# Kernel tuning notes

Hardware: AMD Instinct MI355X
Metric: run time of the kernel (lower is better)

Reference implementation:

```python
import jax, jax.numpy as jnp
import numpy as np

N_NODES = 100000
N_EDGES = 1600000
N_GRAPHS = 256
HIDDEN = 256
ADD_FEATURES = 7
BN_EPS = 1e-5


def setup_inputs() -> dict:
    key = jax.random.key(0)
    ks = jax.random.split(key, 12)
    x = jax.random.normal(ks[0], (N_NODES, 1), dtype=jnp.float32)
    edge_index = jax.random.randint(ks[1], (2, N_EDGES), 0, N_NODES, dtype=jnp.int32)
    batch = jnp.sort(jax.random.randint(ks[2], (N_NODES,), 0, N_GRAPHS, dtype=jnp.int32))
    y_feat = jax.random.normal(ks[3], (N_GRAPHS, ADD_FEATURES), dtype=jnp.float32)
    # learned parameters
    W_conv = jax.random.normal(ks[4], (1, HIDDEN), dtype=jnp.float32) * 0.5
    b_conv = jnp.zeros((HIDDEN,), dtype=jnp.float32)
    gamma = jnp.ones((HIDDEN,), dtype=jnp.float32)
    beta = jnp.zeros((HIDDEN,), dtype=jnp.float32)
    W1 = jax.random.normal(ks[5], (HIDDEN + ADD_FEATURES, 128), dtype=jnp.float32) * (1.0 / np.sqrt(HIDDEN + ADD_FEATURES))
    b1 = jnp.zeros((128,), dtype=jnp.float32)
    W2 = jax.random.normal(ks[6], (128, 2), dtype=jnp.float32) * (1.0 / np.sqrt(128))
    b2 = jnp.zeros((2,), dtype=jnp.float32)
    return {"x": x, "edge_index": edge_index, "batch": batch, "y_feat": y_feat,
            "W_conv": W_conv, "b_conv": b_conv, "gamma": gamma, "beta": beta,
            "W1": W1, "b1": b1, "W2": W2, "b2": b2}


def _gcn_conv(x, W, b, edge_index, n_nodes):
    # PyG GCNConv: add self-loops, symmetric normalization D^-1/2 (A+I) D^-1/2 (x W) + b
    loop = jnp.arange(n_nodes, dtype=edge_index.dtype)
    src = jnp.concatenate([edge_index[0], loop])
    dst = jnp.concatenate([edge_index[1], loop])
    deg = jax.ops.segment_sum(jnp.ones_like(dst, dtype=x.dtype), dst, num_segments=n_nodes)
    dinv = jnp.where(deg > 0, jax.lax.rsqrt(jnp.maximum(deg, 1e-12)), 0.0)
    norm = dinv[src] * dinv[dst]                      # [E+N]
    xw = x @ W                                        # [N, H]
    msg = xw[src] * norm[:, None]                     # gather [E+N, H]
    return jax.ops.segment_sum(msg, dst, num_segments=n_nodes) + b


def reference(x, edge_index, batch, y_feat, W_conv, b_conv, gamma, beta, W1, b1, W2, b2):
    n_nodes = x.shape[0]
    h = _gcn_conv(x, W_conv, b_conv, edge_index, n_nodes)      # [N, 256]
    h = jax.nn.gelu(h, approximate=False)
    # BatchNorm over nodes (training-mode batch stats, biased variance, eps=1e-5)
    mean = jnp.mean(h, axis=0)
    var = jnp.mean(jnp.square(h - mean), axis=0)
    h = (h - mean) * jax.lax.rsqrt(var + BN_EPS) * gamma + beta
    # global mean pool by graph id
    sums = jax.ops.segment_sum(h, batch, num_segments=N_GRAPHS)           # [G, 256]
    counts = jax.ops.segment_sum(jnp.ones((n_nodes,), h.dtype), batch, num_segments=N_GRAPHS)
    pooled = sums / jnp.maximum(counts, 1.0)[:, None]
    g = jnp.concatenate([pooled, y_feat], axis=1)               # [G, 263]
    g = jax.nn.gelu(g @ W1 + b1, approximate=False)             # [G, 128]
    out = jax.nn.sigmoid(g @ W2 + b2)                           # [G, 2]
    return out
```

## Files before the change

### kernel.cpp

```cpp
#include <hip/hip_runtime.h>
#include <hip/hip_bf16.h>

#define HID 256
#define ADDF 7
#define MLP1 128
#define BN_EPS 1e-5f
#define NREP 8

#define NB 512
#define BW 196
#define BCAP 4096
#define PC 2048
#define NW 4

__device__ __forceinline__ float gelu_fast(float z) {
    float z2 = z * z;
    float y2 = z * fmaf(0.07135481627f, z2, 1.59576912161f);
    float u  = __expf(fminf(y2, 80.0f));
    return z * u * __builtin_amdgcn_rcpf(u + 1.0f);
}

__global__ __launch_bounds__(256) void k_hist(
        const int* __restrict__ dst, int* __restrict__ hist,
        float* __restrict__ zbase, int zcount, int E, int nchunk, int cpx) {
    __shared__ int h[NW][NB];
    const int t = threadIdx.x;
    const int bid = blockIdx.x;

    int gt = bid * 256 + t;
    if (gt < zcount) zbase[gt] = 0.0f;

    const int m = (bid & 7) * cpx + (bid >> 3);
    for (int k = t; k < NW * NB; k += 256) (&h[0][0])[k] = 0;
    __syncthreads();

    if (m < nchunk) {
        const int s0 = m * PC;
        const int e0 = min(s0 + PC, E);
        const int w = t >> 6;
        const bool al = ((((uintptr_t)(dst + s0)) & 15) == 0);
        const int n4 = al ? ((e0 - s0) >> 2) : 0;
        const int4* dst4 = (const int4*)(dst + s0);
        for (int q = t; q < n4; q += 256) {
            int4 d = dst4[q];
            atomicAdd(&h[w][d.x / BW], 1);
            atomicAdd(&h[w][d.y / BW], 1);
            atomicAdd(&h[w][d.z / BW], 1);
            atomicAdd(&h[w][d.w / BW], 1);
        }
        for (int i = s0 + (n4 << 2) + t; i < e0; i += 256)
            atomicAdd(&h[w][dst[i] / BW], 1);
        __syncthreads();
        for (int b = t; b < NB; b += 256)
            hist[(size_t)m * NB + b] = h[0][b] + h[1][b] + h[2][b] + h[3][b];
    }
}

__global__ __launch_bounds__(64) void k_scan(
        int* __restrict__ hist, int* __restrict__ binCur,
        const int* __restrict__ batch, int* __restrict__ cnt,
        int nchunk, int N, int G) {
    const int bin = blockIdx.x;
    const int lane = threadIdx.x;
    __shared__ int bounds[2];

    if (bin < G && lane < 2) {
        int target = bin + lane;
        int lo = 0, hi = N;
        while (lo < hi) { int mid = (lo + hi) >> 1; if (batch[mid] < target) lo = mid + 1; else hi = mid; }
        bounds[lane] = lo;
    }

    const int per = (nchunk + 63) / 64;
    const int m0 = lane * per;
    const int m1 = min(m0 + per, nchunk);
    int sum = 0;
    for (int m = m0; m < m1; ++m) sum += hist[(size_t)m * NB + bin];

    int incl = sum;
    #pragma unroll
    for (int d = 1; d < 64; d <<= 1) {
        int o = __shfl_up(incl, d);
        if (lane >= d) incl += o;
    }
    const int total = __shfl(incl, 63);
    int run = bin * BCAP + (incl - sum);
    for (int m = m0; m < m1; ++m) {
        int c = hist[(size_t)m * NB + bin];
        hist[(size_t)m * NB + bin] = run;
        run += c;
    }
    if (lane == 63) binCur[bin] = bin * BCAP + total;

    __syncthreads();
    if (bin < G && lane == 0) cnt[bin] = bounds[1] - bounds[0];
}

__global__ __launch_bounds__(256) void k_store(
        const int* __restrict__ src, const int* __restrict__ dst,
        const int* __restrict__ hist, int* __restrict__ recs,
        int E, int nchunk, int cpx) {
    __shared__ int cur[NB];
    const int t = threadIdx.x;
    const int m = ((int)blockIdx.x & 7) * cpx + ((int)blockIdx.x >> 3);
    if (m >= nchunk) return;

    for (int b = t; b < NB; b += 256) cur[b] = hist[(size_t)m * NB + b];
    __syncthreads();

    const int s0 = m * PC;
    const int e0 = min(s0 + PC, E);
    const bool al = (((((uintptr_t)(dst + s0)) | ((uintptr_t)(src + s0))) & 15) == 0);
    const int n4 = al ? ((e0 - s0) >> 2) : 0;
    const int4* dst4 = (const int4*)(dst + s0);
    const int4* src4 = (const int4*)(src + s0);
    for (int q = t; q < n4; q += 256) {
        int4 d = dst4[q];
        int4 s = src4[q];
        int bin, pos;
        bin = d.x / BW; pos = atomicAdd(&cur[bin], 1); recs[pos] = ((d.x - bin * BW) << 17) | s.x;
        bin = d.y / BW; pos = atomicAdd(&cur[bin], 1); recs[pos] = ((d.y - bin * BW) << 17) | s.y;
        bin = d.z / BW; pos = atomicAdd(&cur[bin], 1); recs[pos] = ((d.z - bin * BW) << 17) | s.z;
        bin = d.w / BW; pos = atomicAdd(&cur[bin], 1); recs[pos] = ((d.w - bin * BW) << 17) | s.w;
    }
    for (int i = s0 + (n4 << 2) + t; i < e0; i += 256) {
        int d = dst[i];
        int bin = d / BW;
        int pos = atomicAdd(&cur[bin], 1);
        recs[pos] = ((d - bin * BW) << 17) | src[i];
    }
}

__global__ __launch_bounds__(512) void k_degv(
        const int* __restrict__ recs, const int* __restrict__ binCur,
        const float* __restrict__ x, float* __restrict__ dinv, float* __restrict__ v, int N) {
    __shared__ int degL[BW];
    const int b = blockIdx.x;
    const int t = threadIdx.x;
    if (t < BW) degL[t] = 0;
    __syncthreads();

    const int start = b * BCAP;
    const int end   = binCur[b];
    const int n4 = (end - start) >> 2;
    const int4* r4 = (const int4*)(recs + start);
    for (int q = t; q < n4; q += 512) {
        int4 r = r4[q];
        atomicAdd(&degL[r.x >> 17], 1);
        atomicAdd(&degL[r.y >> 17], 1);
        atomicAdd(&degL[r.z >> 17], 1);
        atomicAdd(&degL[r.w >> 17], 1);
    }
    for (int i = start + (n4 << 2) + t; i < end; i += 512)
        atomicAdd(&degL[recs[i] >> 17], 1);
    __syncthreads();

    int node = b * BW + t;
    if (t < BW && node < N) {
        float di = rsqrtf((float)degL[t] + 1.0f);
        dinv[node] = di;
        v[node]    = di * x[node];
    }
}

__global__ __launch_bounds__(512) void k_agg_gelu(
        const int* __restrict__ recs, const int* __restrict__ binCur,
        const float* __restrict__ v, const float* __restrict__ dinv,
        const int* __restrict__ batch,
        const float* __restrict__ Wc, const float* __restrict__ bc,
        float* __restrict__ Sgj, float* __restrict__ Trep, float* __restrict__ T2rep, int N) {
    __shared__ float aggL[BW];
    __shared__ float sh_s[BW];
    __shared__ int   sh_b[BW];
    const int b = blockIdx.x;
    const int t = threadIdx.x;
    if (t < BW) aggL[t] = 0.0f;
    __syncthreads();

    const int start = b * BCAP;
    const int end   = binCur[b];
    const int n4 = (end - start) >> 2;
    const int4* r4 = (const int4*)(recs + start);
    for (int q = t; q < n4; q += 512) {
        int4 r = r4[q];
        atomicAdd(&aggL[r.x >> 17], v[r.x & 0x1FFFF]);
        atomicAdd(&aggL[r.y >> 17], v[r.y & 0x1FFFF]);
        atomicAdd(&aggL[r.z >> 17], v[r.z & 0x1FFFF]);
        atomicAdd(&aggL[r.w >> 17], v[r.w & 0x1FFFF]);
    }
    for (int i = start + (n4 << 2) + t; i < end; i += 512) {
        int rec = recs[i];
        atomicAdd(&aggL[rec >> 17], v[rec & 0x1FFFF]);
    }
    __syncthreads();

    const int node0 = b * BW;
    const int count = min(BW, N - node0);
    if (count <= 0) return;

    if (t < count) {
        int node = node0 + t;
        sh_s[t] = dinv[node] * (aggL[t] + v[node]);
        sh_b[t] = batch[node];
    }
    __syncthreads();

    const int f = t & 255;
    const int nbeg = (t < 256) ? 0 : 98;
    const int nend = (t < 256) ? min(98, count) : count;
    if (nbeg < nend) {
        const float wa = Wc[f];
        const float wb = bc[f];
        float tsum = 0.f, t2sum = 0.f, gsum = 0.f;
        int gid = sh_b[nbeg];
        int n = nbeg;
        for (; n + 2 <= nend; n += 2) {
            float h0 = gelu_fast(fmaf(sh_s[n],     wa, wb));
            float h1 = gelu_fast(fmaf(sh_s[n + 1], wa, wb));
            int b0 = sh_b[n], b1v = sh_b[n + 1];
            tsum += h0 + h1; t2sum += fmaf(h0, h0, h1 * h1);
            if (b0 != gid)  { atomicAdd(&Sgj[gid * HID + f], gsum); gsum = 0.f; gid = b0; }
            gsum += h0;
            if (b1v != gid) { atomicAdd(&Sgj[gid * HID + f], gsum); gsum = 0.f; gid = b1v; }
            gsum += h1;
        }
        if (n < nend) {
            float h0 = gelu_fast(fmaf(sh_s[n], wa, wb));
            tsum += h0; t2sum += h0 * h0;
            int b0 = sh_b[n];
            if (b0 != gid) { atomicAdd(&Sgj[gid * HID + f], gsum); gsum = 0.f; gid = b0; }
            gsum += h0;
        }
        atomicAdd(&Sgj[gid * HID + f], gsum);
        const int r = b & (NREP - 1);
        atomicAdd(&Trep [r * HID + f], tsum);
        atomicAdd(&T2rep[r * HID + f], t2sum);
    }
}

__global__ __launch_bounds__(HID) void k_pool_mlp(
        const float* __restrict__ Sgj, const float* __restrict__ Trep, const float* __restrict__ T2rep,
        const int* __restrict__ cnt, const float* __restrict__ gamma, const float* __restrict__ beta,
        const float* __restrict__ yfeat,
        const float* __restrict__ W1, const float* __restrict__ b1,
        const float* __restrict__ W2, const float* __restrict__ b2,
        float* __restrict__ out, int N) {
    __shared__ float gv[HID + ADDF];
    __shared__ float hid[MLP1];
    const int g = blockIdx.x;
    const int t = threadIdx.x;

    float Ts = 0.f, T2s = 0.f;
    #pragma unroll
    for (int r = 0; r < NREP; ++r) { Ts += Trep[r * HID + t]; T2s += T2rep[r * HID + t]; }
    float invN = 1.0f / (float)N;
    float mean = Ts * invN;
    float var  = fmaf(-mean, mean, T2s * invN);
    float rinv = rsqrtf(var + BN_EPS);
    float c = (float)max(cnt[g], 1);
    gv[t] = (Sgj[g * HID + t] / c - mean) * rinv * gamma[t] + beta[t];
    if (t < ADDF) gv[HID + t] = yfeat[g * ADDF + t];
    __syncthreads();

    if (t < MLP1) {
        float acc = b1[t];
        #pragma unroll 8
        for (int k = 0; k < HID + ADDF; ++k)
            acc = fmaf(gv[k], W1[k * MLP1 + t], acc);
        hid[t] = gelu_fast(acc);
    }
    __syncthreads();

    if (t < 2) {
        float o = b2[t];
        for (int k = 0; k < MLP1; ++k)
            o = fmaf(hid[k], W2[k * 2 + t], o);
        out[g * 2 + t] = 1.0f / (1.0f + expf(-o));
    }
}

__global__ void k_init_fb(float* zp, int nz, const int* __restrict__ batch,
                          int* __restrict__ cnt, int N, int G) {
    const int nzBlocks = (nz + 255) / 256;
    if ((int)blockIdx.x < nzBlocks) {
        int i = blockIdx.x * 256 + threadIdx.x;
        if (i < nz) zp[i] = 0.0f;
    } else {
        const int t = threadIdx.x;
        if (t < G) {
            int lo = 0, hi = N;
            while (lo < hi) { int mid = (lo + hi) >> 1; if (batch[mid] < t) lo = mid + 1; else hi = mid; }
            int start = lo;
            lo = 0; hi = N;
            while (lo < hi) { int mid = (lo + hi) >> 1; if (batch[mid] < t + 1) lo = mid + 1; else hi = mid; }
            cnt[t] = lo - start;
        }
    }
}
__global__ void k_zero(float* p, int n) {
    for (int i = blockIdx.x * blockDim.x + threadIdx.x; i < n; i += gridDim.x * blockDim.x)
        p[i] = 0.0f;
}
__global__ void k_deg_fb(const int* __restrict__ dst, float* __restrict__ deg, int E) {
    int i = blockIdx.x * blockDim.x + threadIdx.x;
    if (i < E) atomicAdd(&deg[dst[i]], 1.0f);
}
__global__ void k_dinv_fb(float* __restrict__ deg, const float* __restrict__ x,
                          float* __restrict__ v, int N) {
    int i = blockIdx.x * blockDim.x + threadIdx.x;
    if (i < N) { float di = rsqrtf(deg[i] + 1.0f); deg[i] = di; v[i] = di * x[i]; }
}
__global__ void k_scatter_fb(const int* __restrict__ src, const int* __restrict__ dst,
                             const float* __restrict__ v, float* __restrict__ agg, int E) {
    int i = blockIdx.x * blockDim.x + threadIdx.x;
    if (i < E) atomicAdd(&agg[dst[i]], v[src[i]]);
}
#define CHUNK_FB 64
__global__ __launch_bounds__(HID) void k_gelu_fb(
        const float* __restrict__ v, const float* __restrict__ dinv,
        const float* __restrict__ agg, const int* __restrict__ batch,
        const float* __restrict__ Wc, const float* __restrict__ bc,
        float* __restrict__ Sgj, float* __restrict__ Trep, float* __restrict__ T2rep, int N) {
    __shared__ float sh_s[CHUNK_FB];
    __shared__ int   sh_b[CHUNK_FB];
    const int j = threadIdx.x;
    const int base = blockIdx.x * CHUNK_FB;
    const int count = min(CHUNK_FB, N - base);
    if (j < count) {
        int i = base + j;
        sh_s[j] = dinv[i] * (agg[i] + v[i]);
        sh_b[j] = batch[i];
    }
    __syncthreads();
    const float a = Wc[j];
    const float b = bc[j];
    float tsum = 0.f, t2sum = 0.f, gsum = 0.f;
    int gid = sh_b[0];
    for (int n = 0; n < count; ++n) {
        float h = gelu_fast(fmaf(sh_s[n], a, b));
        tsum += h; t2sum += h * h;
        int bg = sh_b[n];
        if (bg != gid) { atomicAdd(&Sgj[gid * HID + j], gsum); gsum = 0.f; gid = bg; }
        gsum += h;
    }
    atomicAdd(&Sgj[gid * HID + j], gsum);
    const int r = blockIdx.x & (NREP - 1);
    atomicAdd(&Trep [r * HID + j], tsum);
    atomicAdd(&T2rep[r * HID + j], t2sum);
}

extern "C" void kernel_launch(void* const* d_in, const int* in_sizes, int n_in,
                              void* d_out, int out_size, void* d_ws, size_t ws_size,
                              hipStream_t stream) {
    const float* x     = (const float*)d_in[0];
    const int*   edge  = (const int*)  d_in[1];
    const int*   batch = (const int*)  d_in[2];
    const float* yfeat = (const float*)d_in[3];
    const float* Wc    = (const float*)d_in[4];
    const float* bc    = (const float*)d_in[5];
    const float* gamma = (const float*)d_in[6];
    const float* beta  = (const float*)d_in[7];
    const float* W1    = (const float*)d_in[8];
    const float* b1    = (const float*)d_in[9];
    const float* W2    = (const float*)d_in[10];
    const float* b2    = (const float*)d_in[11];
    float* out = (float*)d_out;

    const int N = in_sizes[0];
    const int E = in_sizes[1] / 2;
    const int G = in_sizes[3] / ADDF;

    const int* srcIdx = edge;
    const int* dstIdx = edge + E;

    const int nchunk = (E + PC - 1) / PC;
    const int cpx    = (nchunk + 7) / 8;
    const int pgrid  = cpx * 8;

    float* ws     = (float*)d_ws;
    float* Sgj    = ws;
    float* Trep   = Sgj + (size_t)G * HID;
    float* T2rep  = Trep + NREP * HID;
    int*   cnt    = (int*)(T2rep + NREP * HID);
    int*   binCur = cnt + G;
    float* dinv   = (float*)(binCur + NB);
    float* v      = dinv + (size_t)NB * BW;
    int*   hist   = (int*)(v + (size_t)NB * BW);
    int*   recs   = hist + (size_t)pgrid * NB;

    const size_t headF  = (size_t)G * HID + 2 * NREP * HID + G + NB + 2 * (size_t)NB * BW;
    const size_t needT1 = (headF + (size_t)pgrid * NB + (size_t)NB * BCAP) * 4;
    const int zeroCount = G * HID + 2 * NREP * HID;

    if (ws_size >= needT1 && N <= NB * BW && G <= NB) {
        k_hist<<<pgrid, 256, 0, stream>>>(dstIdx, hist, Sgj, zeroCount, E, nchunk, cpx);
        k_scan<<<NB, 64, 0, stream>>>(hist, binCur, batch, cnt, nchunk, N, G);
        k_store<<<pgrid, 256, 0, stream>>>(srcIdx, dstIdx, hist, recs, E, nchunk, cpx);
        k_degv<<<NB, 512, 0, stream>>>(recs, binCur, x, dinv, v, N);
        k_agg_gelu<<<NB, 512, 0, stream>>>(recs, binCur, v, dinv, batch, Wc, bc, Sgj, Trep, T2rep, N);
        k_pool_mlp<<<G, HID, 0, stream>>>(Sgj, Trep, T2rep, cnt, gamma, beta, yfeat, W1, b1, W2, b2, out, N);
    } else {
        float* degA = (float*)(binCur + NB);
        float* vA   = degA + N;
        float* aggA = vA + N;
        const int initBlocks = (zeroCount + 255) / 256 + 1;
        k_init_fb<<<initBlocks, 256, 0, stream>>>(Sgj, zeroCount, batch, cnt, N, G);
        k_zero<<<512, 256, 0, stream>>>(degA, N);
        k_zero<<<512, 256, 0, stream>>>(aggA, N);
        k_deg_fb<<<(E + 255) / 256, 256, 0, stream>>>(dstIdx, degA, E);
        k_dinv_fb<<<(N + 255) / 256, 256, 0, stream>>>(degA, x, vA, N);
        k_scatter_fb<<<(E + 255) / 256, 256, 0, stream>>>(srcIdx, dstIdx, vA, aggA, E);
        k_gelu_fb<<<(N + CHUNK_FB - 1) / CHUNK_FB, HID, 0, stream>>>(vA, degA, aggA, batch, Wc, bc, Sgj, Trep, T2rep, N);
        k_pool_mlp<<<G, HID, 0, stream>>>(Sgj, Trep, T2rep, cnt, gamma, beta, yfeat, W1, b1, W2, b2, out, N);
    }
}
```

Baseline: 76.88 us.

## Replicate shared-memory accumulators in degree/aggregation kernels and double partition chunk size

The degree and aggregation kernels now keep four copies of their LDS accumulator arrays, one per group of 128 threads, and sum the copies after the scatter. This is meant to reduce same-address contention among the LDS atomics. PC doubles, halving the number of edge chunks and hist rows, and the zeroing of zbase becomes grid-strided so it still covers everything with fewer blocks. k_store also loads its per-chunk hist row with int4 vector loads. With larger chunks each block handles more edges, so fewer blocks are in flight and the hist/store phases have less parallelism.

```diff
diff --git a/kernel.cpp b/kernel.cpp
--- a/kernel.cpp
+++ b/kernel.cpp
@@ -10,8 +10,9 @@
 #define NB 512
 #define BW 196
 #define BCAP 4096
-#define PC 2048
+#define PC 4096
 #define NW 4
+#define NR 4
 
 __device__ __forceinline__ float gelu_fast(float z) {
     float z2 = z * z;
@@ -27,8 +28,7 @@
     const int t = threadIdx.x;
     const int bid = blockIdx.x;
 
-    int gt = bid * 256 + t;
-    if (gt < zcount) zbase[gt] = 0.0f;
+    for (int gt = bid * 256 + t; gt < zcount; gt += (int)gridDim.x * 256) zbase[gt] = 0.0f;
 
     const int m = (bid & 7) * cpx + (bid >> 3);
     for (int k = t; k < NW * NB; k += 256) (&h[0][0])[k] = 0;
@@ -105,7 +105,11 @@
     const int m = ((int)blockIdx.x & 7) * cpx + ((int)blockIdx.x >> 3);
     if (m >= nchunk) return;
 
-    for (int b = t; b < NB; b += 256) cur[b] = hist[(size_t)m * NB + b];
+    {
+        const int4* hrow = (const int4*)(hist + (size_t)m * NB);
+        int4* cur4 = (int4*)cur;
+        for (int b = t; b < NB / 4; b += 256) cur4[b] = hrow[b];
+    }
     __syncthreads();
 
     const int s0 = m * PC;
@@ -134,10 +138,11 @@
 __global__ __launch_bounds__(512) void k_degv(
         const int* __restrict__ recs, const int* __restrict__ binCur,
         const float* __restrict__ x, float* __restrict__ dinv, float* __restrict__ v, int N) {
-    __shared__ int degL[BW];
+    __shared__ int degL[NR][BW];
     const int b = blockIdx.x;
     const int t = threadIdx.x;
-    if (t < BW) degL[t] = 0;
+    const int rp = t >> 7;
+    for (int k = t; k < NR * BW; k += 512) (&degL[0][0])[k] = 0;
     __syncthreads();
 
     const int start = b * BCAP;
@@ -146,18 +151,19 @@
     const int4* r4 = (const int4*)(recs + start);
     for (int q = t; q < n4; q += 512) {
         int4 r = r4[q];
-        atomicAdd(&degL[r.x >> 17], 1);
-        atomicAdd(&degL[r.y >> 17], 1);
-        atomicAdd(&degL[r.z >> 17], 1);
-        atomicAdd(&degL[r.w >> 17], 1);
+        atomicAdd(&degL[rp][r.x >> 17], 1);
+        atomicAdd(&degL[rp][r.y >> 17], 1);
+        atomicAdd(&degL[rp][r.z >> 17], 1);
+        atomicAdd(&degL[rp][r.w >> 17], 1);
     }
     for (int i = start + (n4 << 2) + t; i < end; i += 512)
-        atomicAdd(&degL[recs[i] >> 17], 1);
+        atomicAdd(&degL[rp][recs[i] >> 17], 1);
     __syncthreads();
 
     int node = b * BW + t;
     if (t < BW && node < N) {
-        float di = rsqrtf((float)degL[t] + 1.0f);
+        int d = degL[0][t] + degL[1][t] + degL[2][t] + degL[3][t];
+        float di = rsqrtf((float)d + 1.0f);
         dinv[node] = di;
         v[node]    = di * x[node];
     }
@@ -169,12 +175,13 @@
         const int* __restrict__ batch,
         const float* __restrict__ Wc, const float* __restrict__ bc,
         float* __restrict__ Sgj, float* __restrict__ Trep, float* __restrict__ T2rep, int N) {
-    __shared__ float aggL[BW];
+    __shared__ float aggL[NR][BW];
     __shared__ float sh_s[BW];
     __shared__ int   sh_b[BW];
     const int b = blockIdx.x;
     const int t = threadIdx.x;
-    if (t < BW) aggL[t] = 0.0f;
+    const int rp = t >> 7;
+    for (int k = t; k < NR * BW; k += 512) (&aggL[0][0])[k] = 0.0f;
     __syncthreads();
 
     const int start = b * BCAP;
@@ -183,14 +190,14 @@
     const int4* r4 = (const int4*)(recs + start);
     for (int q = t; q < n4; q += 512) {
         int4 r = r4[q];
-        atomicAdd(&aggL[r.x >> 17], v[r.x & 0x1FFFF]);
-        atomicAdd(&aggL[r.y >> 17], v[r.y & 0x1FFFF]);
-        atomicAdd(&aggL[r.z >> 17], v[r.z & 0x1FFFF]);
-        atomicAdd(&aggL[r.w >> 17], v[r.w & 0x1FFFF]);
+        atomicAdd(&aggL[rp][r.x >> 17], v[r.x & 0x1FFFF]);
+        atomicAdd(&aggL[rp][r.y >> 17], v[r.y & 0x1FFFF]);
+        atomicAdd(&aggL[rp][r.z >> 17], v[r.z & 0x1FFFF]);
+        atomicAdd(&aggL[rp][r.w >> 17], v[r.w & 0x1FFFF]);
     }
     for (int i = start + (n4 << 2) + t; i < end; i += 512) {
         int rec = recs[i];
-        atomicAdd(&aggL[rec >> 17], v[rec & 0x1FFFF]);
+        atomicAdd(&aggL[rp][rec >> 17], v[rec & 0x1FFFF]);
     }
     __syncthreads();
 
@@ -200,7 +207,8 @@
 
     if (t < count) {
         int node = node0 + t;
-        sh_s[t] = dinv[node] * (aggL[t] + v[node]);
+        float a = aggL[0][t] + aggL[1][t] + aggL[2][t] + aggL[3][t];
+        sh_s[t] = dinv[node] * (a + v[node]);
         sh_b[t] = batch[node];
     }
     __syncthreads();
```

After: 72.68 us. -5.5%, faster.
